# Kernel optimization log

Hardware: AMD Instinct MI355X
Metric: run time of the kernel (lower is better)

## Reference

```python
import jax, jax.numpy as jnp
import numpy as np

INPUT_SIZE = 128
HIDDEN_SIZE = 512
OUTPUT_SIZE = 128
NUM_LAYERS = 2
BATCH = 256
SEQ_LEN = 512

def _xavier(key, shape):
    fan_out, fan_in = shape
    limit = jnp.sqrt(6.0 / (fan_in + fan_out))
    return jax.random.uniform(key, shape, jnp.float32, -limit, limit)

def setup_inputs() -> dict:
    key = jax.random.key(0)
    ks = jax.random.split(key, 8)
    x = jax.random.normal(ks[0], (BATCH, SEQ_LEN, INPUT_SIZE), jnp.float32)
    hidden = jnp.zeros((NUM_LAYERS, BATCH, HIDDEN_SIZE), jnp.float32)
    W_ih0 = _xavier(ks[1], (HIDDEN_SIZE, INPUT_SIZE))
    W_hh0 = _xavier(ks[2], (HIDDEN_SIZE, HIDDEN_SIZE))
    W_ih1 = _xavier(ks[3], (HIDDEN_SIZE, HIDDEN_SIZE))
    W_hh1 = _xavier(ks[4], (HIDDEN_SIZE, HIDDEN_SIZE))
    b_ih0 = jnp.zeros((HIDDEN_SIZE,), jnp.float32)
    b_hh0 = jnp.zeros((HIDDEN_SIZE,), jnp.float32)
    b_ih1 = jnp.zeros((HIDDEN_SIZE,), jnp.float32)
    b_hh1 = jnp.zeros((HIDDEN_SIZE,), jnp.float32)
    fc_W = _xavier(ks[5], (OUTPUT_SIZE, HIDDEN_SIZE))
    fc_b = jnp.zeros((OUTPUT_SIZE,), jnp.float32)
    return {"x": x, "hidden": hidden,
            "W_ih0": W_ih0, "b_ih0": b_ih0, "W_hh0": W_hh0, "b_hh0": b_hh0,
            "W_ih1": W_ih1, "b_ih1": b_ih1, "W_hh1": W_hh1, "b_hh1": b_hh1,
            "fc_W": fc_W, "fc_b": fc_b}

def _run_layer(seq_tbi, h0, W_ih, b_ih, W_hh, b_hh):
    # seq_tbi: [T, B, I]; h0: [B, H]
    # Precompute input projection for all timesteps (one big GEMM).
    xin = jnp.einsum('tbi,hi->tbh', seq_tbi, W_ih) + b_ih + b_hh  # [T, B, H]
    def step(h, xt):
        h = jnp.tanh(xt + h @ W_hh.T)
        return h, h
    h_last, outs = jax.lax.scan(step, h0, xin)
    return h_last, outs  # outs: [T, B, H]

def reference(x, hidden, W_ih0, b_ih0, W_hh0, b_hh0, W_ih1, b_ih1, W_hh1, b_hh1, fc_W, fc_b):
    seq = jnp.transpose(x, (1, 0, 2))  # [T, B, I]
    h0_last, out0 = _run_layer(seq, hidden[0], W_ih0, b_ih0, W_hh0, b_hh0)
    h1_last, out1 = _run_layer(out0, hidden[1], W_ih1, b_ih1, W_hh1, b_hh1)
    new_hidden = jnp.stack([h0_last, h1_last], axis=0)  # [L, B, H]
    last_hidden = out1[-1]  # [B, H]
    output = last_hidden @ fc_W.T + fc_b  # [B, O]
    return output, new_hidden
```

## Files before the change

kernel.cpp:

```cpp
#include <hip/hip_runtime.h>

#define NB 256
#define NT 512
#define NI 128
#define NH 512
#define NO 128
#define NGRP 16
#define RPG 16
#define BPG 8

typedef __attribute__((ext_vector_type(8))) __bf16 bf16x8;
typedef __attribute__((ext_vector_type(4))) float  f32x4;
typedef unsigned long long u64;

#define MFMA16(a,b,c) __builtin_amdgcn_mfma_f32_16x16x32_bf16((a),(b),(c),0,0,0)

#define XSZ   (RPG*NI*2)
#define HSZ   (RPG*NH*2)
#define XOFF  0
#define H0OFF (2*XSZ)
#define H1OFF (H0OFF + 2*HSZ)
#define SMEM_BYTES (H1OFF + 2*HSZ)

#define SLABU   2048
#define DATAU   (8*NGRP*SLABU)

union U64x8 { uint4 q[4]; u64 v[8]; };
union U32x8 { uint4 q[2]; unsigned g[8]; };

__device__ __forceinline__ float fast_tanh(float x){
  x = fminf(15.f, fmaxf(-15.f, x));
  float e = __expf(2.f * x);
  return 1.f - 2.f / (e + 1.f);
}

__device__ __forceinline__ bf16x8 cvt8(float4 a, float4 b){
  bf16x8 r;
  r[0]=(__bf16)a.x; r[1]=(__bf16)a.y; r[2]=(__bf16)a.z; r[3]=(__bf16)a.w;
  r[4]=(__bf16)b.x; r[5]=(__bf16)b.y; r[6]=(__bf16)b.z; r[7]=(__bf16)b.w;
  return r;
}

__device__ __forceinline__ bf16x8 loadWfrag(const float* __restrict__ W, int ldk, int row, int k0){
  const float4* p = (const float4*)(W + (size_t)row * ldk + k0);
  return cvt8(p[0], p[1]);
}

__device__ __forceinline__ void st_u64(u64* p, u64 v){
  __hip_atomic_store(p, v, __ATOMIC_RELAXED, __HIP_MEMORY_SCOPE_AGENT);
}
__device__ __forceinline__ u64 ld_u64(const u64* p){
  return __hip_atomic_load(p, __ATOMIC_RELAXED, __HIP_MEMORY_SCOPE_AGENT);
}
__device__ __forceinline__ void st_u32(unsigned* p, unsigned v){
  __hip_atomic_store(p, v, __ATOMIC_RELAXED, __HIP_MEMORY_SCOPE_AGENT);
}
__device__ __forceinline__ unsigned ld_u32(const unsigned* p){
  return __hip_atomic_load(p, __ATOMIC_RELAXED, __HIP_MEMORY_SCOPE_AGENT);
}

__device__ __forceinline__ u64 pack4bf(f32x4 v){
  union { __bf16 h[4]; u64 u; } un;
  un.h[0]=(__bf16)v[0]; un.h[1]=(__bf16)v[1]; un.h[2]=(__bf16)v[2]; un.h[3]=(__bf16)v[3];
  return un.u;
}

__device__ __forceinline__ unsigned cksum(unsigned tick, u64 d){
  return tick + (unsigned)d + (unsigned)(d >> 32);
}

__device__ __forceinline__ u64* slabD(u64* b, int l, int p, int g){
  return b + ((size_t)(((l << 2) | p) * NGRP + g)) * SLABU;
}
__device__ __forceinline__ unsigned* slabT(unsigned* b, int l, int p, int g){
  return b + ((size_t)(((l << 2) | p) * NGRP + g)) * SLABU;
}

__global__ __launch_bounds__(256, 1)
void rnn_persistent(const float* __restrict__ x,
                    const float* __restrict__ hid,
                    const float* __restrict__ Wih0, const float* __restrict__ bih0,
                    const float* __restrict__ Whh0, const float* __restrict__ bhh0,
                    const float* __restrict__ Wih1, const float* __restrict__ bih1,
                    const float* __restrict__ Whh1, const float* __restrict__ bhh1,
                    const float* __restrict__ fcW,  const float* __restrict__ fcb,
                    float* __restrict__ out,
                    u64* __restrict__ ex)
{
  __shared__ __align__(16) char smem[SMEM_BYTES];

  const int tid  = threadIdx.x;
  const int lane = tid & 63;
  const int wv   = tid >> 6;
  const int lr   = lane & 15;
  const int lq   = lane >> 4;

  const int bq  = blockIdx.x;
  const int j   = (bq >> 3) & 7;
  const int g   = (bq & 7) + 8 * (bq >> 6);
  const int cb  = j * 64 + wv * 16;
  const int row0 = g * RPG;
  const int idxp = j * 256 + wv * 64 + lane;

  u64* const dat = ex;
  unsigned* const tag = (unsigned*)(ex + DATAU);

  bf16x8 wih0[4], whh0[16], wih1[16], whh1[16];
#pragma unroll
  for (int kt = 0; kt < 4;  ++kt) wih0[kt] = loadWfrag(Wih0, NI, cb + lr, kt*32 + lq*8);
#pragma unroll
  for (int kt = 0; kt < 16; ++kt) whh0[kt] = loadWfrag(Whh0, NH, cb + lr, kt*32 + lq*8);
#pragma unroll
  for (int kt = 0; kt < 16; ++kt) wih1[kt] = loadWfrag(Wih1, NH, cb + lr, kt*32 + lq*8);
#pragma unroll
  for (int kt = 0; kt < 16; ++kt) whh1[kt] = loadWfrag(Whh1, NH, cb + lr, kt*32 + lq*8);

  const f32x4 bias0 = *(const f32x4*)(bih0 + cb + lq*4) + *(const f32x4*)(bhh0 + cb + lq*4);
  const f32x4 bias1 = *(const f32x4*)(bih1 + cb + lq*4) + *(const f32x4*)(bhh1 + cb + lq*4);

  {
    int r = tid >> 4, i0 = (tid & 15) * 8;
    const float4* xp = (const float4*)(x + ((size_t)(row0 + r) * NT + 0) * NI + i0);
    bf16x8 v = cvt8(xp[0], xp[1]);
    int o = r * 256 + i0 * 2;
    *(bf16x8*)(smem + XOFF + (o ^ ((r & 7) << 4))) = v;
  }
#pragma unroll
  for (int it = 0; it < 4; ++it) {
    int e = it * 2048 + tid * 8;
    int r = e >> 9, c = e & 511;
    int o = r * 1024 + c * 2;
    const float4* hp0 = (const float4*)(hid + (size_t)(row0 + r) * NH + c);
    *(bf16x8*)(smem + H0OFF + (o ^ ((r & 7) << 4))) = cvt8(hp0[0], hp0[1]);
    const float4* hp1 = (const float4*)(hid + (size_t)NB * NH + (size_t)(row0 + r) * NH + c);
    *(bf16x8*)(smem + H1OFF + HSZ + (o ^ ((r & 7) << 4))) = cvt8(hp1[0], hp1[1]);
  }
  __syncthreads();

#define HFRAG(base, kt) (*(const bf16x8*)((base) + lr * 1024 + (((kt) * 64 + lq * 16) ^ ((lr & 7) << 4))))

#define LOAD8(V, G, D, T)                                                              \
  { _Pragma("unroll") for (int i_ = 0; i_ < 8; ++i_) V[i_] = ld_u64((D) + tid*8 + i_); \
    _Pragma("unroll") for (int i_ = 0; i_ < 8; ++i_) G[i_] = ld_u32((T) + tid*8 + i_); }

#define CHECK8(OK, V, G, TICK)                                                         \
  { OK = true;                                                                         \
    _Pragma("unroll") for (int i_ = 0; i_ < 8; ++i_)                                   \
      OK &= (G[i_] == cksum((TICK), V[i_])); }

#define FASTLOAD8(V, G, D, T)                                                          \
  { const uint4* P_ = (const uint4*)((const char*)(D) + (size_t)tid * 64);             \
    const uint4* Q_ = (const uint4*)((const char*)(T) + (size_t)tid * 32);             \
    U64x8 U_; U_.q[0]=P_[0]; U_.q[1]=P_[1]; U_.q[2]=P_[2]; U_.q[3]=P_[3];              \
    U32x8 G_; G_.q[0]=Q_[0]; G_.q[1]=Q_[1];                                            \
    _Pragma("unroll") for (int i_ = 0; i_ < 8; ++i_) { V[i_]=U_.v[i_]; G[i_]=G_.g[i_]; } }

#define RESTAGE8(BASE, V)                                                              \
  { _Pragma("unroll") for (int i_ = 0; i_ < 8; ++i_) {                                 \
      int o_ = ((tid & 1) * 8 + i_) * 1024 + (tid >> 1) * 8;                           \
      *(u64*)((BASE) + (o_ ^ (i_ << 4))) = V[i_]; } }

  for (int t = 0; t <= NT; ++t) {
    const char* xA  = smem + XOFF  + (t & 1) * XSZ;
    const char* h0A = smem + H0OFF + (t & 1) * HSZ;
    const char* h1A = smem + H1OFF + (t & 1) * HSZ;
    char* h0N = smem + H0OFF + ((t + 1) & 1) * HSZ;
    char* h1N = smem + H1OFF + ((t + 1) & 1) * HSZ;
    const bool do0 = (t < NT), do1 = (t > 0);
    const unsigned tick = (unsigned)(t + 1);
    const int par = t & 3;

    u64*      D0 = slabD(dat, 0, par, g);
    unsigned* T0 = slabT(tag, 0, par, g);
    u64*      D1 = slabD(dat, 1, par, g);
    unsigned* T1 = slabT(tag, 1, par, g);

    if (do0) {
      f32x4 a0={0.f,0.f,0.f,0.f}, a1={0.f,0.f,0.f,0.f};
#pragma unroll
      for (int kt = 0; kt < 4; ++kt) {
        bf16x8 a = *(const bf16x8*)(xA + lr * 256 + ((kt * 64 + lq * 16) ^ ((lr & 7) << 4)));
        a0 = MFMA16(wih0[kt], a, a0);
      }
#pragma unroll
      for (int kt = 0; kt < 16; ++kt) {
        bf16x8 a = HFRAG(h0A, kt);
        if (kt & 1) a1 = MFMA16(whh0[kt], a, a1); else a0 = MFMA16(whh0[kt], a, a0);
      }
      f32x4 s = a0 + a1 + bias0;
      f32x4 h; h[0]=fast_tanh(s[0]); h[1]=fast_tanh(s[1]); h[2]=fast_tanh(s[2]); h[3]=fast_tanh(s[3]);
      if (t == NT - 1)
        *(f32x4*)(out + NB * NO + (size_t)(row0 + lr) * NH + cb + lq * 4) = h;
      u64 d = pack4bf(h);
      st_u64(D0 + idxp, d);
      st_u32(T0 + idxp, cksum(tick, d));
    }

    if (do1) {
      f32x4 c0={0.f,0.f,0.f,0.f}, c1={0.f,0.f,0.f,0.f};
#pragma unroll
      for (int kt = 0; kt < 16; ++kt) {
        bf16x8 a = HFRAG(h0A, kt);
        if (kt & 1) c1 = MFMA16(wih1[kt], a, c1); else c0 = MFMA16(wih1[kt], a, c0);
      }
#pragma unroll
      for (int kt = 0; kt < 16; ++kt) {
        bf16x8 a = HFRAG(h1A, kt);
        if (kt & 1) c1 = MFMA16(whh1[kt], a, c1); else c0 = MFMA16(whh1[kt], a, c0);
      }
      f32x4 s = c0 + c1 + bias1;
      f32x4 h; h[0]=fast_tanh(s[0]); h[1]=fast_tanh(s[1]); h[2]=fast_tanh(s[2]); h[3]=fast_tanh(s[3]);
      if (t == NT)
        *(f32x4*)(out + NB * NO + (size_t)NB * NH + (size_t)(row0 + lr) * NH + cb + lq * 4) = h;
      u64 d = pack4bf(h);
      st_u64(D1 + idxp, d);
      st_u32(T1 + idxp, cksum(tick, d));
    }
    if (t == NT) break;

    float4 xr0, xr1;
    const bool xpf = (t + 1 < NT);
    if (xpf) {
      int r = tid >> 4, i0 = (tid & 15) * 8;
      const float4* xp = (const float4*)(x + ((size_t)(row0 + r) * NT + (t + 1)) * NI + i0);
      xr0 = xp[0]; xr1 = xp[1];
    }

    {
      u64 v0[8]; unsigned g0[8];
      FASTLOAD8(v0, g0, D0, T0);
      bool ok; CHECK8(ok, v0, g0, tick);
      while (!ok) { LOAD8(v0, g0, D0, T0); CHECK8(ok, v0, g0, tick); }
      RESTAGE8(h0N, v0);
    }
    if (do1) {
      u64 v1[8]; unsigned g1[8];
      FASTLOAD8(v1, g1, D1, T1);
      bool ok; CHECK8(ok, v1, g1, tick);
      while (!ok) { LOAD8(v1, g1, D1, T1); CHECK8(ok, v1, g1, tick); }
      RESTAGE8(h1N, v1);
    }

    if (xpf) {
      int r = tid >> 4, i0 = (tid & 15) * 8;
      bf16x8 v = cvt8(xr0, xr1);
      char* dst = smem + XOFF + ((t + 1) & 1) * XSZ;
      *(bf16x8*)(dst + ((r * 256 + i0 * 2) ^ ((r & 7) << 4))) = v;
    }
    __syncthreads();
  }

  {
    u64*      DF = slabD(dat, 1, NT & 3, g);
    unsigned* TF = slabT(tag, 1, NT & 3, g);
    u64 vf[8]; unsigned gf[8];
    FASTLOAD8(vf, gf, DF, TF);
    bool ok; CHECK8(ok, vf, gf, (unsigned)(NT + 1));
    while (!ok) { LOAD8(vf, gf, DF, TF); CHECK8(ok, vf, gf, (unsigned)(NT + 1)); }
    char* hF = smem + H1OFF + HSZ;
    RESTAGE8(hF, vf);
    __syncthreads();
  }
  if (wv == 0) {
    const char* hF = smem + H1OFF + HSZ;
    f32x4 acc = {0.f,0.f,0.f,0.f};
#pragma unroll
    for (int kt = 0; kt < 16; ++kt) {
      bf16x8 b = HFRAG(hF, kt);
      bf16x8 a = loadWfrag(fcW, NH, j * 16 + lr, kt * 32 + lq * 8);
      acc = MFMA16(a, b, acc);
    }
    f32x4 fb = *(const f32x4*)(fcb + j * 16 + lq * 4);
    *(f32x4*)(out + (size_t)(row0 + lr) * NO + j * 16 + lq * 4) = acc + fb;
  }
#undef RESTAGE8
#undef FASTLOAD8
#undef CHECK8
#undef LOAD8
#undef HFRAG
}

extern "C" void kernel_launch(void* const* d_in, const int* in_sizes, int n_in,
                              void* d_out, int out_size, void* d_ws, size_t ws_size,
                              hipStream_t stream)
{
  const float* x    = (const float*)d_in[0];
  const float* hid  = (const float*)d_in[1];
  const float* Wih0 = (const float*)d_in[2];
  const float* bih0 = (const float*)d_in[3];
  const float* Whh0 = (const float*)d_in[4];
  const float* bhh0 = (const float*)d_in[5];
  const float* Wih1 = (const float*)d_in[6];
  const float* bih1 = (const float*)d_in[7];
  const float* Whh1 = (const float*)d_in[8];
  const float* bhh1 = (const float*)d_in[9];
  const float* fcW  = (const float*)d_in[10];
  const float* fcb  = (const float*)d_in[11];
  float* out = (float*)d_out;

  u64* ex = (u64*)d_ws;

  (void)hipMemsetAsync(d_ws, 0, (size_t)3 * 1024 * 1024, stream);

  hipLaunchKernelGGL(rnn_persistent, dim3(NGRP * BPG), dim3(256), 0, stream,
                     x, hid, Wih0, bih0, Whh0, bhh0, Wih1, bih1, Whh1, bhh1,
                     fcW, fcb, out, ex);
}
```

Before: 1.885 ms.

## Add per-group flag barrier before polling exchange slabs and widen slab ring

Each wave now publishes a per-step tick flag after its exchange stores have drained (s_waitcnt vmcnt(0)). Before reading the exchanged hidden-state slabs, every wave spins on its group's 32 flags instead of repeatedly polling the full data+checksum slabs. The slab ring depth becomes a runtime parameter, 8 when the workspace is large enough and 4 otherwise, which enlarges the memset. This adds a full store drain and an extra flag round-trip on the per-timestep critical path, in exchange for lighter polling traffic.

```diff
diff --git a/kernel.cpp b/kernel.cpp
--- a/kernel.cpp
+++ b/kernel.cpp
@@ -23,7 +23,6 @@
 #define SMEM_BYTES (H1OFF + 2*HSZ)
 
 #define SLABU   2048
-#define DATAU   (8*NGRP*SLABU)
 
 union U64x8 { uint4 q[4]; u64 v[8]; };
 union U32x8 { uint4 q[2]; unsigned g[8]; };
@@ -67,13 +66,6 @@
 
 __device__ __forceinline__ unsigned cksum(unsigned tick, u64 d){
   return tick + (unsigned)d + (unsigned)(d >> 32);
-}
-
-__device__ __forceinline__ u64* slabD(u64* b, int l, int p, int g){
-  return b + ((size_t)(((l << 2) | p) * NGRP + g)) * SLABU;
-}
-__device__ __forceinline__ unsigned* slabT(unsigned* b, int l, int p, int g){
-  return b + ((size_t)(((l << 2) | p) * NGRP + g)) * SLABU;
 }
 
 __global__ __launch_bounds__(256, 1)
@@ -85,7 +77,10 @@
                     const float* __restrict__ Whh1, const float* __restrict__ bhh1,
                     const float* __restrict__ fcW,  const float* __restrict__ fcb,
                     float* __restrict__ out,
-                    u64* __restrict__ ex)
+                    unsigned* __restrict__ flags,
+                    u64* __restrict__ dat,
+                    unsigned* __restrict__ tag,
+                    int NP)
 {
   __shared__ __align__(16) char smem[SMEM_BYTES];
 
@@ -100,10 +95,14 @@
   const int g   = (bq & 7) + 8 * (bq >> 6);
   const int cb  = j * 64 + wv * 16;
   const int row0 = g * RPG;
+  const int wid  = j * 4 + wv;
   const int idxp = j * 256 + wv * 64 + lane;
-
-  u64* const dat = ex;
-  unsigned* const tag = (unsigned*)(ex + DATAU);
+  const int pmask = NP - 1;
+
+#define SLABD(l, p) (dat + ((size_t)(((l)*NP + (p)) * NGRP + g)) * SLABU)
+#define SLABT(l, p) (tag + ((size_t)(((l)*NP + (p)) * NGRP + g)) * SLABU)
+
+  unsigned* flg = flags + g * 64;
 
   bf16x8 wih0[4], whh0[16], wih1[16], whh1[16];
 #pragma unroll
@@ -168,12 +167,12 @@
     char* h1N = smem + H1OFF + ((t + 1) & 1) * HSZ;
     const bool do0 = (t < NT), do1 = (t > 0);
     const unsigned tick = (unsigned)(t + 1);
-    const int par = t & 3;
-
-    u64*      D0 = slabD(dat, 0, par, g);
-    unsigned* T0 = slabT(tag, 0, par, g);
-    u64*      D1 = slabD(dat, 1, par, g);
-    unsigned* T1 = slabT(tag, 1, par, g);
+    const int par = t & pmask;
+
+    u64*      D0 = SLABD(0, par);
+    unsigned* T0 = SLABT(0, par);
+    u64*      D1 = SLABD(1, par);
+    unsigned* T1 = SLABT(1, par);
 
     if (do0) {
       f32x4 a0={0.f,0.f,0.f,0.f}, a1={0.f,0.f,0.f,0.f};
@@ -216,6 +215,9 @@
       st_u64(D1 + idxp, d);
       st_u32(T1 + idxp, cksum(tick, d));
     }
+
+    asm volatile("s_waitcnt vmcnt(0)" ::: "memory");
+    if (lane == 0) st_u32(flg + wid, tick);
     if (t == NT) break;
 
     float4 xr0, xr1;
@@ -227,6 +229,15 @@
     }
 
     {
+      const int need = (int)tick;
+      for (;;) {
+        unsigned f = ld_u32(flg + (lane & 31));
+        if (__all((int)f - need >= 0)) break;
+      }
+      asm volatile("" ::: "memory");
+    }
+
+    {
       u64 v0[8]; unsigned g0[8];
       FASTLOAD8(v0, g0, D0, T0);
       bool ok; CHECK8(ok, v0, g0, tick);
@@ -251,8 +262,16 @@
   }
 
   {
-    u64*      DF = slabD(dat, 1, NT & 3, g);
-    unsigned* TF = slabT(tag, 1, NT & 3, g);
+    const int need = NT + 1;
+    for (;;) {
+      unsigned f = ld_u32(flg + (lane & 31));
+      if (__all((int)f - need >= 0)) break;
+    }
+    asm volatile("" ::: "memory");
+  }
+  {
+    u64*      DF = SLABD(1, NT & pmask);
+    unsigned* TF = SLABT(1, NT & pmask);
     u64 vf[8]; unsigned gf[8];
     FASTLOAD8(vf, gf, DF, TF);
     bool ok; CHECK8(ok, vf, gf, (unsigned)(NT + 1));
@@ -278,6 +297,8 @@
 #undef CHECK8
 #undef LOAD8
 #undef HFRAG
+#undef SLABT
+#undef SLABD
 }
 
 extern "C" void kernel_launch(void* const* d_in, const int* in_sizes, int n_in,
@@ -298,11 +319,16 @@
   const float* fcb  = (const float*)d_in[11];
   float* out = (float*)d_out;
 
-  u64* ex = (u64*)d_ws;
-
-  (void)hipMemsetAsync(d_ws, 0, (size_t)3 * 1024 * 1024, stream);
+  int NP = (ws_size >= (size_t)(65536 + 8 * 768 * 1024)) ? 8 : 4;
+  size_t need = (size_t)65536 + (size_t)NP * 768 * 1024;
+
+  unsigned* flags = (unsigned*)d_ws;
+  u64*      dat   = (u64*)((char*)d_ws + 65536);
+  unsigned* tagp  = (unsigned*)((char*)d_ws + 65536 + (size_t)NP * 512 * 1024);
+
+  (void)hipMemsetAsync(d_ws, 0, need, stream);
 
   hipLaunchKernelGGL(rnn_persistent, dim3(NGRP * BPG), dim3(256), 0, stream,
                      x, hid, Wih0, bih0, Whh0, bhh0, Wih1, bih1, Whh1, bhh1,
-                     fcW, fcb, out, ex);
-}
+                     fcW, fcb, out, flags, dat, tagp, NP);
+}
```

Measured after the change: 2.401 ms. +27.4%, slower.

## Warp-specialize persistent RNN: split compute waves from spin-ingest waves

Applied to the files above, without the earlier changes.

Doubles the block to 512 threads. Waves 0-3 hold the weight fragments and run both layers' MFMA steps plus the x prefetch. Waves 4-7 only spin on the cross-block tag/checksum slabs and restage the arriving hidden state into shared memory. The goal is to take polling latency off the compute waves and overlap it with local work. The cost is extra waves contending for the CU, while the per-step dependency chain still goes through global-memory exchange.

```diff
diff --git a/kernel.cpp b/kernel.cpp
--- a/kernel.cpp
+++ b/kernel.cpp
@@ -8,6 +8,7 @@
 #define NGRP 16
 #define RPG 16
 #define BPG 8
+#define NPAR 4
 
 typedef __attribute__((ext_vector_type(8))) __bf16 bf16x8;
 typedef __attribute__((ext_vector_type(4))) float  f32x4;
@@ -23,7 +24,6 @@
 #define SMEM_BYTES (H1OFF + 2*HSZ)
 
 #define SLABU   2048
-#define DATAU   (8*NGRP*SLABU)
 
 union U64x8 { uint4 q[4]; u64 v[8]; };
 union U32x8 { uint4 q[2]; unsigned g[8]; };
@@ -69,14 +69,7 @@
   return tick + (unsigned)d + (unsigned)(d >> 32);
 }
 
-__device__ __forceinline__ u64* slabD(u64* b, int l, int p, int g){
-  return b + ((size_t)(((l << 2) | p) * NGRP + g)) * SLABU;
-}
-__device__ __forceinline__ unsigned* slabT(unsigned* b, int l, int p, int g){
-  return b + ((size_t)(((l << 2) | p) * NGRP + g)) * SLABU;
-}
-
-__global__ __launch_bounds__(256, 1)
+__global__ __launch_bounds__(512, 2)
 void rnn_persistent(const float* __restrict__ x,
                     const float* __restrict__ hid,
                     const float* __restrict__ Wih0, const float* __restrict__ bih0,
@@ -85,7 +78,8 @@
                     const float* __restrict__ Whh1, const float* __restrict__ bhh1,
                     const float* __restrict__ fcW,  const float* __restrict__ fcb,
                     float* __restrict__ out,
-                    u64* __restrict__ ex)
+                    u64* __restrict__ dat,
+                    unsigned* __restrict__ tag)
 {
   __shared__ __align__(16) char smem[SMEM_BYTES];
 
@@ -98,50 +92,55 @@
   const int bq  = blockIdx.x;
   const int j   = (bq >> 3) & 7;
   const int g   = (bq & 7) + 8 * (bq >> 6);
-  const int cb  = j * 64 + wv * 16;
+  const int cb  = j * 64 + (wv & 3) * 16;
   const int row0 = g * RPG;
-  const int idxp = j * 256 + wv * 64 + lane;
-
-  u64* const dat = ex;
-  unsigned* const tag = (unsigned*)(ex + DATAU);
+  const int idxp = j * 256 + (wv & 3) * 64 + lane;
+  const int it   = tid & 255;
+
+#define SLABD(l, p) (dat + ((size_t)(((l)*NPAR + (p)) * NGRP + g)) * SLABU)
+#define SLABT(l, p) (tag + ((size_t)(((l)*NPAR + (p)) * NGRP + g)) * SLABU)
 
   bf16x8 wih0[4], whh0[16], wih1[16], whh1[16];
-#pragma unroll
-  for (int kt = 0; kt < 4;  ++kt) wih0[kt] = loadWfrag(Wih0, NI, cb + lr, kt*32 + lq*8);
-#pragma unroll
-  for (int kt = 0; kt < 16; ++kt) whh0[kt] = loadWfrag(Whh0, NH, cb + lr, kt*32 + lq*8);
-#pragma unroll
-  for (int kt = 0; kt < 16; ++kt) wih1[kt] = loadWfrag(Wih1, NH, cb + lr, kt*32 + lq*8);
-#pragma unroll
-  for (int kt = 0; kt < 16; ++kt) whh1[kt] = loadWfrag(Whh1, NH, cb + lr, kt*32 + lq*8);
-
-  const f32x4 bias0 = *(const f32x4*)(bih0 + cb + lq*4) + *(const f32x4*)(bhh0 + cb + lq*4);
-  const f32x4 bias1 = *(const f32x4*)(bih1 + cb + lq*4) + *(const f32x4*)(bhh1 + cb + lq*4);
-
-  {
-    int r = tid >> 4, i0 = (tid & 15) * 8;
-    const float4* xp = (const float4*)(x + ((size_t)(row0 + r) * NT + 0) * NI + i0);
-    bf16x8 v = cvt8(xp[0], xp[1]);
-    int o = r * 256 + i0 * 2;
-    *(bf16x8*)(smem + XOFF + (o ^ ((r & 7) << 4))) = v;
-  }
-#pragma unroll
-  for (int it = 0; it < 4; ++it) {
-    int e = it * 2048 + tid * 8;
-    int r = e >> 9, c = e & 511;
-    int o = r * 1024 + c * 2;
-    const float4* hp0 = (const float4*)(hid + (size_t)(row0 + r) * NH + c);
-    *(bf16x8*)(smem + H0OFF + (o ^ ((r & 7) << 4))) = cvt8(hp0[0], hp0[1]);
-    const float4* hp1 = (const float4*)(hid + (size_t)NB * NH + (size_t)(row0 + r) * NH + c);
-    *(bf16x8*)(smem + H1OFF + HSZ + (o ^ ((r & 7) << 4))) = cvt8(hp1[0], hp1[1]);
+  f32x4 bias0 = {0.f,0.f,0.f,0.f}, bias1 = {0.f,0.f,0.f,0.f};
+  if (wv < 4) {
+#pragma unroll
+    for (int kt = 0; kt < 4;  ++kt) wih0[kt] = loadWfrag(Wih0, NI, cb + lr, kt*32 + lq*8);
+#pragma unroll
+    for (int kt = 0; kt < 16; ++kt) whh0[kt] = loadWfrag(Whh0, NH, cb + lr, kt*32 + lq*8);
+#pragma unroll
+    for (int kt = 0; kt < 16; ++kt) wih1[kt] = loadWfrag(Wih1, NH, cb + lr, kt*32 + lq*8);
+#pragma unroll
+    for (int kt = 0; kt < 16; ++kt) whh1[kt] = loadWfrag(Whh1, NH, cb + lr, kt*32 + lq*8);
+    bias0 = *(const f32x4*)(bih0 + cb + lq*4) + *(const f32x4*)(bhh0 + cb + lq*4);
+    bias1 = *(const f32x4*)(bih1 + cb + lq*4) + *(const f32x4*)(bhh1 + cb + lq*4);
+  }
+
+  if (tid < 256) {
+    {
+      int r = tid >> 4, i0 = (tid & 15) * 8;
+      const float4* xp = (const float4*)(x + ((size_t)(row0 + r) * NT + 0) * NI + i0);
+      bf16x8 v = cvt8(xp[0], xp[1]);
+      int o = r * 256 + i0 * 2;
+      *(bf16x8*)(smem + XOFF + (o ^ ((r & 7) << 4))) = v;
+    }
+#pragma unroll
+    for (int itr = 0; itr < 4; ++itr) {
+      int e = itr * 2048 + tid * 8;
+      int r = e >> 9, c = e & 511;
+      int o = r * 1024 + c * 2;
+      const float4* hp0 = (const float4*)(hid + (size_t)(row0 + r) * NH + c);
+      *(bf16x8*)(smem + H0OFF + (o ^ ((r & 7) << 4))) = cvt8(hp0[0], hp0[1]);
+      const float4* hp1 = (const float4*)(hid + (size_t)NB * NH + (size_t)(row0 + r) * NH + c);
+      *(bf16x8*)(smem + H1OFF + HSZ + (o ^ ((r & 7) << 4))) = cvt8(hp1[0], hp1[1]);
+    }
   }
   __syncthreads();
 
 #define HFRAG(base, kt) (*(const bf16x8*)((base) + lr * 1024 + (((kt) * 64 + lq * 16) ^ ((lr & 7) << 4))))
 
 #define LOAD8(V, G, D, T)                                                              \
-  { _Pragma("unroll") for (int i_ = 0; i_ < 8; ++i_) V[i_] = ld_u64((D) + tid*8 + i_); \
-    _Pragma("unroll") for (int i_ = 0; i_ < 8; ++i_) G[i_] = ld_u32((T) + tid*8 + i_); }
+  { _Pragma("unroll") for (int i_ = 0; i_ < 8; ++i_) V[i_] = ld_u64((D) + it*8 + i_);  \
+    _Pragma("unroll") for (int i_ = 0; i_ < 8; ++i_) G[i_] = ld_u32((T) + it*8 + i_); }
 
 #define CHECK8(OK, V, G, TICK)                                                         \
   { OK = true;                                                                         \
@@ -149,16 +148,23 @@
       OK &= (G[i_] == cksum((TICK), V[i_])); }
 
 #define FASTLOAD8(V, G, D, T)                                                          \
-  { const uint4* P_ = (const uint4*)((const char*)(D) + (size_t)tid * 64);             \
-    const uint4* Q_ = (const uint4*)((const char*)(T) + (size_t)tid * 32);             \
+  { const uint4* P_ = (const uint4*)((const char*)(D) + (size_t)it * 64);              \
+    const uint4* Q_ = (const uint4*)((const char*)(T) + (size_t)it * 32);              \
     U64x8 U_; U_.q[0]=P_[0]; U_.q[1]=P_[1]; U_.q[2]=P_[2]; U_.q[3]=P_[3];              \
     U32x8 G_; G_.q[0]=Q_[0]; G_.q[1]=Q_[1];                                            \
     _Pragma("unroll") for (int i_ = 0; i_ < 8; ++i_) { V[i_]=U_.v[i_]; G[i_]=G_.g[i_]; } }
 
 #define RESTAGE8(BASE, V)                                                              \
   { _Pragma("unroll") for (int i_ = 0; i_ < 8; ++i_) {                                 \
-      int o_ = ((tid & 1) * 8 + i_) * 1024 + (tid >> 1) * 8;                           \
+      int o_ = ((it & 1) * 8 + i_) * 1024 + (it >> 1) * 8;                             \
       *(u64*)((BASE) + (o_ ^ (i_ << 4))) = V[i_]; } }
+
+#define SPIN_INGEST(DST, D, T, TICK)                                                   \
+  { u64 v_[8]; unsigned g_[8]; bool ok_;                                               \
+    FASTLOAD8(v_, g_, D, T);                                                           \
+    CHECK8(ok_, v_, g_, TICK);                                                         \
+    while (!ok_) { LOAD8(v_, g_, D, T); CHECK8(ok_, v_, g_, TICK); }                   \
+    RESTAGE8(DST, v_); }
 
   for (int t = 0; t <= NT; ++t) {
     const char* xA  = smem + XOFF  + (t & 1) * XSZ;
@@ -168,99 +174,68 @@
     char* h1N = smem + H1OFF + ((t + 1) & 1) * HSZ;
     const bool do0 = (t < NT), do1 = (t > 0);
     const unsigned tick = (unsigned)(t + 1);
-    const int par = t & 3;
-
-    u64*      D0 = slabD(dat, 0, par, g);
-    unsigned* T0 = slabT(tag, 0, par, g);
-    u64*      D1 = slabD(dat, 1, par, g);
-    unsigned* T1 = slabT(tag, 1, par, g);
-
-    if (do0) {
-      f32x4 a0={0.f,0.f,0.f,0.f}, a1={0.f,0.f,0.f,0.f};
-#pragma unroll
-      for (int kt = 0; kt < 4; ++kt) {
-        bf16x8 a = *(const bf16x8*)(xA + lr * 256 + ((kt * 64 + lq * 16) ^ ((lr & 7) << 4)));
-        a0 = MFMA16(wih0[kt], a, a0);
+    const int par = t & (NPAR - 1);
+
+    u64*      D0 = SLABD(0, par);
+    unsigned* T0 = SLABT(0, par);
+    u64*      D1 = SLABD(1, par);
+    unsigned* T1 = SLABT(1, par);
+
+    if (wv < 4) {
+      if (do0) {
+        f32x4 a0={0.f,0.f,0.f,0.f}, a1={0.f,0.f,0.f,0.f};
+#pragma unroll
+        for (int kt = 0; kt < 4; ++kt) {
+          bf16x8 a = *(const bf16x8*)(xA + lr * 256 + ((kt * 64 + lq * 16) ^ ((lr & 7) << 4)));
+          a0 = MFMA16(wih0[kt], a, a0);
+        }
+#pragma unroll
+        for (int kt = 0; kt < 16; ++kt) {
+          bf16x8 a = HFRAG(h0A, kt);
+          if (kt & 1) a1 = MFMA16(whh0[kt], a, a1); else a0 = MFMA16(whh0[kt], a, a0);
+        }
+        f32x4 s = a0 + a1 + bias0;
+        f32x4 h; h[0]=fast_tanh(s[0]); h[1]=fast_tanh(s[1]); h[2]=fast_tanh(s[2]); h[3]=fast_tanh(s[3]);
+        if (t == NT - 1)
+          *(f32x4*)(out + NB * NO + (size_t)(row0 + lr) * NH + cb + lq * 4) = h;
+        u64 d = pack4bf(h);
+        st_u64(D0 + idxp, d);
+        st_u32(T0 + idxp, cksum(tick, d));
       }
-#pragma unroll
-      for (int kt = 0; kt < 16; ++kt) {
-        bf16x8 a = HFRAG(h0A, kt);
-        if (kt & 1) a1 = MFMA16(whh0[kt], a, a1); else a0 = MFMA16(whh0[kt], a, a0);
+      if (do1) {
+        f32x4 c0={0.f,0.f,0.f,0.f}, c1={0.f,0.f,0.f,0.f};
+#pragma unroll
+        for (int kt = 0; kt < 16; ++kt) {
+          bf16x8 a = HFRAG(h0A, kt);
+          if (kt & 1) c1 = MFMA16(wih1[kt], a, c1); else c0 = MFMA16(wih1[kt], a, c0);
+        }
+#pragma unroll
+        for (int kt = 0; kt < 16; ++kt) {
+          bf16x8 a = HFRAG(h1A, kt);
+          if (kt & 1) c1 = MFMA16(whh1[kt], a, c1); else c0 = MFMA16(whh1[kt], a, c0);
+        }
+        f32x4 s = c0 + c1 + bias1;
+        f32x4 h; h[0]=fast_tanh(s[0]); h[1]=fast_tanh(s[1]); h[2]=fast_tanh(s[2]); h[3]=fast_tanh(s[3]);
+        if (t == NT)
+          *(f32x4*)(out + NB * NO + (size_t)NB * NH + (size_t)(row0 + lr) * NH + cb + lq * 4) = h;
+        u64 d = pack4bf(h);
+        st_u64(D1 + idxp, d);
+        st_u32(T1 + idxp, cksum(tick, d));
       }
-      f32x4 s = a0 + a1 + bias0;
-      f32x4 h; h[0]=fast_tanh(s[0]); h[1]=fast_tanh(s[1]); h[2]=fast_tanh(s[2]); h[3]=fast_tanh(s[3]);
-      if (t == NT - 1)
-        *(f32x4*)(out + NB * NO + (size_t)(row0 + lr) * NH + cb + lq * 4) = h;
-      u64 d = pack4bf(h);
-      st_u64(D0 + idxp, d);
-      st_u32(T0 + idxp, cksum(tick, d));
-    }
-
-    if (do1) {
-      f32x4 c0={0.f,0.f,0.f,0.f}, c1={0.f,0.f,0.f,0.f};
-#pragma unroll
-      for (int kt = 0; kt < 16; ++kt) {
-        bf16x8 a = HFRAG(h0A, kt);
-        if (kt & 1) c1 = MFMA16(wih1[kt], a, c1); else c0 = MFMA16(wih1[kt], a, c0);
+      if (t + 1 < NT && tid < 256) {
+        int r = tid >> 4, i0 = (tid & 15) * 8;
+        const float4* xp = (const float4*)(x + ((size_t)(row0 + r) * NT + (t + 1)) * NI + i0);
+        bf16x8 v = cvt8(xp[0], xp[1]);
+        char* dst = smem + XOFF + ((t + 1) & 1) * XSZ;
+        *(bf16x8*)(dst + ((r * 256 + i0 * 2) ^ ((r & 7) << 4))) = v;
       }
-#pragma unroll
-      for (int kt = 0; kt < 16; ++kt) {
-        bf16x8 a = HFRAG(h1A, kt);
-        if (kt & 1) c1 = MFMA16(whh1[kt], a, c1); else c0 = MFMA16(whh1[kt], a, c0);
-      }
-      f32x4 s = c0 + c1 + bias1;
-      f32x4 h; h[0]=fast_tanh(s[0]); h[1]=fast_tanh(s[1]); h[2]=fast_tanh(s[2]); h[3]=fast_tanh(s[3]);
-      if (t == NT)
-        *(f32x4*)(out + NB * NO + (size_t)NB * NH + (size_t)(row0 + lr) * NH + cb + lq * 4) = h;
-      u64 d = pack4bf(h);
-      st_u64(D1 + idxp, d);
-      st_u32(T1 + idxp, cksum(tick, d));
-    }
-    if (t == NT) break;
-
-    float4 xr0, xr1;
-    const bool xpf = (t + 1 < NT);
-    if (xpf) {
-      int r = tid >> 4, i0 = (tid & 15) * 8;
-      const float4* xp = (const float4*)(x + ((size_t)(row0 + r) * NT + (t + 1)) * NI + i0);
-      xr0 = xp[0]; xr1 = xp[1];
-    }
-
-    {
-      u64 v0[8]; unsigned g0[8];
-      FASTLOAD8(v0, g0, D0, T0);
-      bool ok; CHECK8(ok, v0, g0, tick);
-      while (!ok) { LOAD8(v0, g0, D0, T0); CHECK8(ok, v0, g0, tick); }
-      RESTAGE8(h0N, v0);
-    }
-    if (do1) {
-      u64 v1[8]; unsigned g1[8];
-      FASTLOAD8(v1, g1, D1, T1);
-      bool ok; CHECK8(ok, v1, g1, tick);
-      while (!ok) { LOAD8(v1, g1, D1, T1); CHECK8(ok, v1, g1, tick); }
-      RESTAGE8(h1N, v1);
-    }
-
-    if (xpf) {
-      int r = tid >> 4, i0 = (tid & 15) * 8;
-      bf16x8 v = cvt8(xr0, xr1);
-      char* dst = smem + XOFF + ((t + 1) & 1) * XSZ;
-      *(bf16x8*)(dst + ((r * 256 + i0 * 2) ^ ((r & 7) << 4))) = v;
+    } else {
+      if (do0) { SPIN_INGEST(h0N, D0, T0, tick); }
+      if (do1) { SPIN_INGEST(h1N, D1, T1, tick); }
     }
     __syncthreads();
   }
 
-  {
-    u64*      DF = slabD(dat, 1, NT & 3, g);
-    unsigned* TF = slabT(tag, 1, NT & 3, g);
-    u64 vf[8]; unsigned gf[8];
-    FASTLOAD8(vf, gf, DF, TF);
-    bool ok; CHECK8(ok, vf, gf, (unsigned)(NT + 1));
-    while (!ok) { LOAD8(vf, gf, DF, TF); CHECK8(ok, vf, gf, (unsigned)(NT + 1)); }
-    char* hF = smem + H1OFF + HSZ;
-    RESTAGE8(hF, vf);
-    __syncthreads();
-  }
   if (wv == 0) {
     const char* hF = smem + H1OFF + HSZ;
     f32x4 acc = {0.f,0.f,0.f,0.f};
@@ -273,11 +248,14 @@
     f32x4 fb = *(const f32x4*)(fcb + j * 16 + lq * 4);
     *(f32x4*)(out + (size_t)(row0 + lr) * NO + j * 16 + lq * 4) = acc + fb;
   }
+#undef SPIN_INGEST
 #undef RESTAGE8
 #undef FASTLOAD8
 #undef CHECK8
 #undef LOAD8
 #undef HFRAG
+#undef SLABT
+#undef SLABD
 }
 
 extern "C" void kernel_launch(void* const* d_in, const int* in_sizes, int n_in,
@@ -298,11 +276,15 @@
   const float* fcb  = (const float*)d_in[11];
   float* out = (float*)d_out;
 
-  u64* ex = (u64*)d_ws;
-
-  (void)hipMemsetAsync(d_ws, 0, (size_t)3 * 1024 * 1024, stream);
-
-  hipLaunchKernelGGL(rnn_persistent, dim3(NGRP * BPG), dim3(256), 0, stream,
+  size_t dbytes = (size_t)NPAR * 512 * 1024;
+  size_t need   = (size_t)NPAR * 768 * 1024;
+
+  u64*      dat  = (u64*)d_ws;
+  unsigned* tagp = (unsigned*)((char*)d_ws + dbytes);
+
+  (void)hipMemsetAsync(d_ws, 0, need, stream);
+
+  hipLaunchKernelGGL(rnn_persistent, dim3(NGRP * BPG), dim3(512), 0, stream,
                      x, hid, Wih0, bih0, Whh0, bhh0, Wih1, bih1, Whh1, bhh1,
-                     fcW, fcb, out, ex);
-}
+                     fcW, fcb, out, dat, tagp);
+}
```

After: 4.951 ms. 163% more time.
